# Performance work log

Hardware: AMD Instinct MI355X
Metric: run time of the kernel (lower is better)

The kernel has to match this reference:

```python
import math
import jax, jax.numpy as jnp
import numpy as np

B, LQ, LK = 4, 1024, 1024
D_MODEL, NHEAD, FFN = 1024, 16, 4096
DEPTH = D_MODEL // NHEAD  # 64
MAX_REL = 1024
EPS = 1e-5


def _rel_embedding():
    # fixed (non-learned) buffer: clamped relative-position indices used as float values
    length = max(MAX_REL, DEPTH)
    r = np.arange(length)
    mat = np.clip(r[None, :] - r[:, None], -MAX_REL, MAX_REL) + MAX_REL
    return jnp.asarray(mat[:MAX_REL, :DEPTH], jnp.float32)  # [MAX_REL, DEPTH]


def _skew(rel, length_k):
    # rel: [B, H, Lq, Lq] -> relative logits aligned to key positions [B, H, Lq, Lk]
    b, h, lq, m = rel.shape
    assert lq == m
    rel = jnp.pad(rel, ((0, 0), (0, 0), (0, 0), (1, 0)))
    rel = rel.reshape(b, h, lq + 1, lq)[:, :, 1:, :]
    if length_k > lq:
        rel = jnp.pad(rel, ((0, 0), (0, 0), (0, 0), (0, length_k - lq)))
    elif length_k < lq:
        rel = rel[:, :, :, :length_k]
    return rel


def _split_heads(t):
    b, l, _ = t.shape
    return t.reshape(b, l, NHEAD, DEPTH).transpose(0, 2, 1, 3)  # [b,h,l,d]


def _rga(x_q, x_kv, Wq, bq, Wo, bo, mask, rel_e):
    # NOTE: faithful to source - Q, K and V all use query_projection
    q = _split_heads(x_q @ Wq + bq)
    k = _split_heads(x_kv @ Wq + bq)
    v = _split_heads(x_kv @ Wq + bq)
    lq, lk = q.shape[2], k.shape[2]
    logits = jnp.einsum('bhqd,bhkd->bhqk', q, k)
    start = max(0, MAX_REL - lq)
    ke = rel_e[start:, :]  # [min(MAX_REL,lq), DEPTH]
    rel = jnp.einsum('bhld,md->bhlm', q, ke)
    logits = (logits + _skew(rel, lk)) / math.sqrt(DEPTH)
    if mask is not None:
        logits = jnp.where(mask, logits, jnp.asarray(-1e9, logits.dtype))
    w = jax.nn.softmax(logits, axis=-1)
    out = jnp.einsum('bhqk,bhkd->bhqd', w, v)
    out = out.transpose(0, 2, 1, 3).reshape(x_q.shape[0], lq, D_MODEL)
    return out @ Wo + bo


def _layernorm(x, g, b):
    mu = jnp.mean(x, axis=-1, keepdims=True)
    var = jnp.mean(jnp.square(x - mu), axis=-1, keepdims=True)
    return (x - mu) * jax.lax.rsqrt(var + EPS) * g + b


def setup_inputs() -> dict:
    key = jax.random.key(0)
    ks = jax.random.split(key, 12)
    s = 0.02
    inp = {
        'tgt': jax.random.normal(ks[0], (B, LQ, D_MODEL), jnp.float32),
        'memory': jax.random.normal(ks[1], (B, LK, D_MODEL), jnp.float32),
        'tgt_mask': jnp.tril(jnp.ones((LQ, LQ), dtype=bool)),
        'sa_Wq': jax.random.normal(ks[2], (D_MODEL, D_MODEL), jnp.float32) * s,
        'sa_bq': jnp.zeros((D_MODEL,), jnp.float32),
        'sa_Wo': jax.random.normal(ks[3], (D_MODEL, D_MODEL), jnp.float32) * s,
        'sa_bo': jnp.zeros((D_MODEL,), jnp.float32),
        'ca_Wq': jax.random.normal(ks[4], (D_MODEL, D_MODEL), jnp.float32) * s,
        'ca_bq': jnp.zeros((D_MODEL,), jnp.float32),
        'ca_Wo': jax.random.normal(ks[5], (D_MODEL, D_MODEL), jnp.float32) * s,
        'ca_bo': jnp.zeros((D_MODEL,), jnp.float32),
        'ffn_W1': jax.random.normal(ks[6], (D_MODEL, FFN), jnp.float32) * s,
        'ffn_b1': jnp.zeros((FFN,), jnp.float32),
        'ffn_W2': jax.random.normal(ks[7], (FFN, D_MODEL), jnp.float32) * s,
        'ffn_b2': jnp.zeros((D_MODEL,), jnp.float32),
        'ln1_g': jnp.ones((D_MODEL,), jnp.float32), 'ln1_b': jnp.zeros((D_MODEL,), jnp.float32),
        'ln2_g': jnp.ones((D_MODEL,), jnp.float32), 'ln2_b': jnp.zeros((D_MODEL,), jnp.float32),
        'ln3_g': jnp.ones((D_MODEL,), jnp.float32), 'ln3_b': jnp.zeros((D_MODEL,), jnp.float32),
    }
    return inp


def reference(tgt, memory, tgt_mask, sa_Wq, sa_bq, sa_Wo, sa_bo, ca_Wq, ca_bq, ca_Wo, ca_bo,
              ffn_W1, ffn_b1, ffn_W2, ffn_b2, ln1_g, ln1_b, ln2_g, ln2_b, ln3_g, ln3_b):
    rel_e = _rel_embedding()
    # self-attention (relative-global) with causal mask
    x = tgt + _rga(tgt, tgt, sa_Wq, sa_bq, sa_Wo, sa_bo, tgt_mask, rel_e)
    x = _layernorm(x, ln1_g, ln1_b)
    # cross-attention (also relative-global per source)
    x = x + _rga(x, memory, ca_Wq, ca_bq, ca_Wo, ca_bo, None, rel_e)
    x = _layernorm(x, ln2_g, ln2_b)
    # FFN
    h = jax.nn.relu(x @ ffn_W1 + ffn_b1)
    x = x + (h @ ffn_W2 + ffn_b2)
    x = _layernorm(x, ln3_g, ln3_b)
    return x
```

## Files before the change

kernel.cpp:

```cpp
#include <hip/hip_runtime.h>

typedef __attribute__((ext_vector_type(4))) float f32x4;
typedef __attribute__((ext_vector_type(8))) short s16x8;
typedef __attribute__((ext_vector_type(4))) unsigned short u16x4;

__device__ __forceinline__ unsigned short f2bf(float x) {
  union { float f; unsigned u; } un; un.f = x;
  unsigned u = un.u;
  u += 0x7FFFu + ((u >> 16) & 1u);
  return (unsigned short)(u >> 16);
}
__device__ __forceinline__ float bf2f(unsigned short h) {
  union { unsigned u; float f; } un; un.u = ((unsigned)h) << 16; return un.f;
}

__device__ __forceinline__ f32x4 mfma16(s16x8 a, s16x8 b, f32x4 c) {
  asm("v_mfma_f32_16x16x32_bf16 %0, %1, %2, %0" : "+v"(c) : "v"(a), "v"(b));
  return c;
}

__device__ __forceinline__ void gld16(const void* g, void* l) {
  __builtin_amdgcn_global_load_lds(
      (const __attribute__((address_space(1))) void*)g,
      (__attribute__((address_space(3))) void*)l, 16, 0, 0);
}

template<bool RELU, bool RESID, bool OUT_BF16>
__global__ __launch_bounds__(256, 2) void bgemm_k(
    const unsigned short* __restrict__ Ab, const unsigned short* __restrict__ Bb,
    const float* __restrict__ bias, const float* __restrict__ resid,
    void* __restrict__ Cp, int M, int N, int K, int lbx)
{
  __shared__ __align__(16) unsigned short As[2][128 * 64];
  __shared__ __align__(16) unsigned short Bs[2][128 * 64];

  const int nwg = gridDim.x;
  const int bid = blockIdx.x;
  const int swz = (bid & 7) * (nwg >> 3) + (bid >> 3);
  const int nbx_m1 = (1 << lbx) - 1;
  const int n0 = (swz & nbx_m1) * 128;
  const int m0 = (swz >> lbx) * 128;

  const int tid = threadIdx.x;
  const int lane = tid & 63;
  const int w = tid >> 6;
  const int wm = w >> 1, wn = w & 1;
  const int li = lane & 15, g = lane >> 4;

  f32x4 acc[4][4] = {};

#define STAGE(buf, kt) do { \
    const int k0_ = (kt) * 64; \
    _Pragma("unroll") \
    for (int i_ = 0; i_ < 4; i_++) { \
      int lin = i_ * 256 + tid; int row = lin >> 3; \
      int cg = (lin & 7) ^ (row & 7); \
      gld16(Ab + (size_t)(m0 + row) * K + k0_ + cg * 8, &As[buf][lin * 8]); \
    } \
    _Pragma("unroll") \
    for (int i_ = 0; i_ < 4; i_++) { \
      int lin = i_ * 256 + tid; int row = lin >> 3; \
      int cg = (lin & 7) ^ (row & 7); \
      gld16(Bb + (size_t)(n0 + row) * K + k0_ + cg * 8, &Bs[buf][lin * 8]); \
    } \
  } while (0)

  const int NT = K >> 6;
  STAGE(0, 0);
  for (int t = 0; t < NT; ++t) {
    const int cur = t & 1;
    if (t + 1 < NT) {
      STAGE(cur ^ 1, t + 1);
      asm volatile("s_waitcnt vmcnt(8)" ::: "memory");
    } else {
      asm volatile("s_waitcnt vmcnt(0)" ::: "memory");
    }
    __builtin_amdgcn_sched_barrier(0);
    __builtin_amdgcn_s_barrier();
    __builtin_amdgcn_sched_barrier(0);
#pragma unroll
    for (int ks = 0; ks < 2; ++ks) {
      s16x8 af[4], bf[4];
#pragma unroll
      for (int mt = 0; mt < 4; mt++) {
        int row = wm * 64 + mt * 16 + li;
        int slot = (4 * ks + g) ^ (row & 7);
        af[mt] = *(const s16x8*)&As[cur][row * 64 + slot * 8];
      }
#pragma unroll
      for (int nt = 0; nt < 4; nt++) {
        int row = wn * 64 + nt * 16 + li;
        int slot = (4 * ks + g) ^ (row & 7);
        bf[nt] = *(const s16x8*)&Bs[cur][row * 64 + slot * 8];
      }
#pragma unroll
      for (int mt = 0; mt < 4; mt++)
#pragma unroll
        for (int nt = 0; nt < 4; nt++)
          acc[mt][nt] = mfma16(af[mt], bf[nt], acc[mt][nt]);
    }
    __builtin_amdgcn_sched_barrier(0);
    __builtin_amdgcn_s_barrier();
    __builtin_amdgcn_sched_barrier(0);
  }
#undef STAGE

  asm volatile("s_nop 7\n\ts_nop 7" :::);
#pragma unroll
  for (int mt = 0; mt < 4; mt++) {
    int mrow = m0 + wm * 64 + mt * 16 + 4 * g;
#pragma unroll
    for (int nt = 0; nt < 4; nt++) {
      int ncol = n0 + wn * 64 + nt * 16 + li;
      float bv = bias ? bias[ncol] : 0.f;
#pragma unroll
      for (int r = 0; r < 4; r++) {
        int mr = mrow + r;
        float v = acc[mt][nt][r] + bv;
        if (RESID) v += resid[(size_t)mr * N + ncol];
        if (RELU) v = fmaxf(v, 0.f);
        if (OUT_BF16) ((unsigned short*)Cp)[(size_t)mr * N + ncol] = f2bf(v);
        else          ((float*)Cp)[(size_t)mr * N + ncol] = v;
      }
    }
  }
}

__global__ __launch_bounds__(256, 2) void sgemm_k(
    const unsigned short* __restrict__ Ah, const unsigned short* __restrict__ Al,
    const unsigned short* __restrict__ A2h, const unsigned short* __restrict__ A2l,
    const unsigned short* __restrict__ Bh, const unsigned short* __restrict__ Bl,
    const float* __restrict__ bias,
    unsigned short* __restrict__ Cb, unsigned short* __restrict__ C2b,
    int Ms, int M, int N, int K, int lbx)
{
  __shared__ __align__(16) unsigned short AsH[128 * 64];
  __shared__ __align__(16) unsigned short AsL[128 * 64];
  __shared__ __align__(16) unsigned short BsH[128 * 64];
  __shared__ __align__(16) unsigned short BsL[128 * 64];

  const int nwg = gridDim.x;
  const int bid = blockIdx.x;
  const int swz = (bid & 7) * (nwg >> 3) + (bid >> 3);
  const int nbx_m1 = (1 << lbx) - 1;
  const int n0 = (swz & nbx_m1) * 128;
  int m0 = (swz >> lbx) * 128;

  const unsigned short* Ahp = Ah;
  const unsigned short* Alp = Al;
  unsigned short* Cp = Cb;
  if (m0 >= Ms) { Ahp = A2h; Alp = A2l; Cp = C2b; m0 -= Ms; }

  const int tid = threadIdx.x;
  const int lane = tid & 63;
  const int w = tid >> 6;
  const int wm = w >> 1, wn = w & 1;
  const int li = lane & 15, g = lane >> 4;

  f32x4 acc[4][4] = {};

  const int NT = K >> 6;
  for (int t = 0; t < NT; ++t) {
    __syncthreads();
#pragma unroll
    for (int i = 0; i < 4; i++) {
      int lin = i * 256 + tid; int row = lin >> 3;
      int cg = (lin & 7) ^ (row & 7);
      size_t offA = (size_t)(m0 + row) * K + t * 64 + cg * 8;
      size_t offB = (size_t)(n0 + row) * K + t * 64 + cg * 8;
      gld16(Ahp + offA, &AsH[lin * 8]);
      gld16(Alp + offA, &AsL[lin * 8]);
      gld16(Bh + offB, &BsH[lin * 8]);
      gld16(Bl + offB, &BsL[lin * 8]);
    }
    asm volatile("s_waitcnt vmcnt(0)" ::: "memory");
    __syncthreads();
#pragma unroll
    for (int ks = 0; ks < 2; ++ks) {
      s16x8 ah[4], al[4], bh[4], bl[4];
#pragma unroll
      for (int mt = 0; mt < 4; mt++) {
        int row = wm * 64 + mt * 16 + li;
        int slot = (4 * ks + g) ^ (row & 7);
        ah[mt] = *(const s16x8*)&AsH[row * 64 + slot * 8];
        al[mt] = *(const s16x8*)&AsL[row * 64 + slot * 8];
      }
#pragma unroll
      for (int nt = 0; nt < 4; nt++) {
        int row = wn * 64 + nt * 16 + li;
        int slot = (4 * ks + g) ^ (row & 7);
        bh[nt] = *(const s16x8*)&BsH[row * 64 + slot * 8];
        bl[nt] = *(const s16x8*)&BsL[row * 64 + slot * 8];
      }
#pragma unroll
      for (int mt = 0; mt < 4; mt++)
#pragma unroll
        for (int nt = 0; nt < 4; nt++) {
          acc[mt][nt] = mfma16(ah[mt], bh[nt], acc[mt][nt]);
          acc[mt][nt] = mfma16(ah[mt], bl[nt], acc[mt][nt]);
          acc[mt][nt] = mfma16(al[mt], bh[nt], acc[mt][nt]);
        }
    }
  }

  asm volatile("s_nop 7\n\ts_nop 7" :::);
#pragma unroll
  for (int mt = 0; mt < 4; mt++) {
    int mrow = m0 + wm * 64 + mt * 16 + 4 * g;
#pragma unroll
    for (int nt = 0; nt < 4; nt++) {
      int ncol = n0 + wn * 64 + nt * 16 + li;
      float bv = bias[ncol];
#pragma unroll
      for (int r = 0; r < 4; r++) {
        int mr = mrow + r;
        Cp[(size_t)mr * N + ncol] = f2bf(acc[mt][nt][r] + bv);
      }
    }
  }
}

__device__ __forceinline__ void dev_tc(const float* __restrict__ W,
    unsigned short* __restrict__ WT, int K, int N, int bid, char* ldsu)
{
  unsigned short (*Ls)[65] = (unsigned short (*)[65])ldsu;
  int ntx = N >> 6;
  int ty = bid / ntx, tx = bid - ty * ntx;
  int r0 = ty << 6, c0 = tx << 6;
  int tid = threadIdx.x;
  int rl = tid >> 4, cl = (tid & 15) << 2;
#pragma unroll
  for (int rr = 0; rr < 4; rr++) {
    f32x4 v = *(const f32x4*)&W[(size_t)(r0 + rl + rr * 16) * N + c0 + cl];
#pragma unroll
    for (int j = 0; j < 4; j++) Ls[rl + rr * 16][cl + j] = f2bf(v[j]);
  }
  __syncthreads();
#pragma unroll
  for (int rr = 0; rr < 4; rr++) {
    int nl = rl + rr * 16;
    u16x4 o;
#pragma unroll
    for (int j = 0; j < 4; j++) o[j] = Ls[cl + j][nl];
    *(u16x4*)&WT[(size_t)(c0 + nl) * K + r0 + cl] = o;
  }
}

__device__ __forceinline__ void dev_tc2(const float* __restrict__ W,
    unsigned short* __restrict__ WTh, unsigned short* __restrict__ WTl,
    int K, int N, int bid, char* ldsu)
{
  float (*Ls)[65] = (float (*)[65])ldsu;
  int ntx = N >> 6;
  int ty = bid / ntx, tx = bid - ty * ntx;
  int r0 = ty << 6, c0 = tx << 6;
  int tid = threadIdx.x;
  int rl = tid >> 4, cl = (tid & 15) << 2;
#pragma unroll
  for (int rr = 0; rr < 4; rr++) {
    f32x4 v = *(const f32x4*)&W[(size_t)(r0 + rl + rr * 16) * N + c0 + cl];
#pragma unroll
    for (int j = 0; j < 4; j++) Ls[rl + rr * 16][cl + j] = v[j];
  }
  __syncthreads();
#pragma unroll
  for (int rr = 0; rr < 4; rr++) {
    int nl = rl + rr * 16;
    u16x4 oh, ol;
#pragma unroll
    for (int j = 0; j < 4; j++) {
      float v = Ls[cl + j][nl];
      unsigned short h = f2bf(v);
      oh[j] = h; ol[j] = f2bf(v - bf2f(h));
    }
    *(u16x4*)&WTh[(size_t)(c0 + nl) * K + r0 + cl] = oh;
    *(u16x4*)&WTl[(size_t)(c0 + nl) * K + r0 + cl] = ol;
  }
}

__global__ __launch_bounds__(256) void prep_w_k(
    const float* saWq, const float* caWq, const float* saWo, const float* caWo,
    const float* W1, const float* W2,
    unsigned short* WqTsaH, unsigned short* WqTsaL,
    unsigned short* WqTcaH, unsigned short* WqTcaL,
    unsigned short* WoTsa, unsigned short* WoTca,
    unsigned short* W1T, unsigned short* W2T)
{
  __shared__ __align__(16) char LDSU[64 * 65 * 4];
  int bid = blockIdx.x;
  if (bid < 256)       dev_tc2(saWq, WqTsaH, WqTsaL, 1024, 1024, bid, LDSU);
  else if (bid < 512)  dev_tc2(caWq, WqTcaH, WqTcaL, 1024, 1024, bid - 256, LDSU);
  else if (bid < 768)  dev_tc (saWo, WoTsa, 1024, 1024, bid - 512, LDSU);
  else if (bid < 1024) dev_tc (caWo, WoTca, 1024, 1024, bid - 768, LDSU);
  else if (bid < 2048) dev_tc (W1, W1T, 1024, 4096, bid - 1024, LDSU);
  else                 dev_tc (W2, W2T, 4096, 1024, bid - 2048, LDSU);
}

__device__ __forceinline__ void dev_cvt2row(const float* __restrict__ X,
    unsigned short* __restrict__ H, unsigned short* __restrict__ L, int bid)
{
  int i = (bid * 256 + threadIdx.x) * 4;
  f32x4 v = *(const f32x4*)&X[i];
  u16x4 hh, ll;
#pragma unroll
  for (int j = 0; j < 4; j++) {
    unsigned short h = f2bf(v[j]);
    hh[j] = h; ll[j] = f2bf(v[j] - bf2f(h));
  }
  *(u16x4*)&H[i] = hh;
  *(u16x4*)&L[i] = ll;
}

__device__ __forceinline__ void dev_wrel(const float* __restrict__ Wq,
    float* __restrict__ Wr, int bid)
{
  int idx = bid * 256 + threadIdx.x;
  int k = idx >> 4, h = idx & 15;
  const float* src = Wq + (size_t)k * 1024 + h * 64;
  float a = 0.f, s = 0.f;
#pragma unroll
  for (int d = 0; d < 64; d += 4) {
    f32x4 v = *(const f32x4*)&src[d];
#pragma unroll
    for (int j = 0; j < 4; j++) { a += v[j] * (float)(d + j + 1024); s += v[j]; }
  }
  Wr[k * 32 + h] = a;
  Wr[k * 32 + 16 + h] = s;
}

__device__ __forceinline__ void dev_crel(const float* __restrict__ bq,
    float* __restrict__ cr)
{
  int h = threadIdx.x;
  if (h < 16) {
    float a = 0.f, s = 0.f;
    for (int d = 0; d < 64; d++) { float v = bq[h * 64 + d]; a += v * (float)(d + 1024); s += v; }
    cr[h] = a; cr[16 + h] = s;
  }
}

__global__ __launch_bounds__(256) void prep_a_k(
    const float* tgt, const float* mem,
    unsigned short* tgth, unsigned short* tgtl,
    unsigned short* memh, unsigned short* meml,
    const float* saWq, const float* caWq, float* wrelsa, float* wrelca,
    const float* sabq, const float* cabq, float* crelsa, float* crelca)
{
  int bid = blockIdx.x;
  if (bid < 4096)       dev_cvt2row(tgt, tgth, tgtl, bid);
  else if (bid < 8192)  dev_cvt2row(mem, memh, meml, bid - 4096);
  else if (bid < 8256)  dev_wrel(saWq, wrelsa, bid - 8192);
  else if (bid < 8320)  dev_wrel(caWq, wrelca, bid - 8256);
  else if (bid == 8320) dev_crel(sabq, crelsa);
  else                  dev_crel(cabq, crelca);
}

__global__ __launch_bounds__(256) void relgemm_k(const float* __restrict__ X,
    const float* __restrict__ Wr, const float* __restrict__ cr,
    float* __restrict__ Out)
{
  __shared__ float Xs[8][256];
  __shared__ float Ws[256][32];
  int r0 = blockIdx.x * 8;
  int tid = threadIdx.x;
  int rl = tid >> 5, col = tid & 31;
  float acc = 0.f;
  for (int kc = 0; kc < 1024; kc += 256) {
    __syncthreads();
    {
      const float* xs = X + (size_t)(r0 + rl) * 1024 + kc + col * 8;
      *(f32x4*)&Xs[rl][col * 8] = *(const f32x4*)xs;
      *(f32x4*)&Xs[rl][col * 8 + 4] = *(const f32x4*)(xs + 4);
    }
    {
      const float* wsrc = Wr + (size_t)(kc + tid) * 32;
#pragma unroll
      for (int i = 0; i < 8; i++) *(f32x4*)&Ws[tid][i * 4] = *(const f32x4*)&wsrc[i * 4];
    }
    __syncthreads();
#pragma unroll 8
    for (int kk = 0; kk < 256; ++kk) acc += Xs[rl][kk] * Ws[kk][col];
  }
  Out[(size_t)(r0 + rl) * 32 + col] = acc + cr[col];
}

template<bool CAUSAL>
__global__ __launch_bounds__(512) void attn_k(
    const unsigned short* __restrict__ Qb, const unsigned short* __restrict__ KVb,
    const float* __restrict__ rAS, unsigned short* __restrict__ Ob)
{
  const int bh = blockIdx.x;
  const int b = bh >> 4, h = bh & 15;
  const int y = blockIdx.y;
  const int tid = threadIdx.x, lane = tid & 63, w = tid >> 6;
  const int g = lane >> 4, li = lane & 15;

  __shared__ __align__(16) unsigned short Kt[64 * 64];
  __shared__ __align__(16) unsigned short KT[64 * 64];
  __shared__ __align__(16) unsigned short Pl[8][16 * 64];

  const int tile = CAUSAL ? ((w < 4) ? y : (15 - y)) : (2 * y + (w >> 2));
  const int q0 = tile * 64 + (w & 3) * 16;
  const int nkb = CAUSAL ? (16 - y) : 16;

  s16x8 qf[2];
  {
    const unsigned short* qrow = Qb + (size_t)(b * 1024 + q0 + li) * 1024 + h * 64;
    qf[0] = *(const s16x8*)&qrow[8 * g];
    qf[1] = *(const s16x8*)&qrow[8 * g + 32];
  }
  const float SCL2 = 0.125f * 1.44269504f;
  int qri[4];
  float C0c[4], C1c[4], rSc[4], rS1c[4];
#pragma unroll
  for (int r = 0; r < 4; r++) {
    int qr = q0 + 4 * g + r;
    qri[r] = qr;
    float rA = rAS[(size_t)(b * 1024 + qr) * 32 + h];
    float rS = rAS[(size_t)(b * 1024 + qr) * 32 + 16 + h];
    int q1 = (qr + 1 < 1024) ? qr + 1 : 1023;
    float rA1 = rAS[(size_t)(b * 1024 + q1) * 32 + h];
    float rS1 = rAS[(size_t)(b * 1024 + q1) * 32 + 16 + h];
    C0c[r]  = (rA + (float)(qr - 1023) * rS) * SCL2;
    rSc[r]  = rS * SCL2;
    C1c[r]  = (rA1 + (float)(qr + 2) * rS1) * SCL2;
    rS1c[r] = rS1 * SCL2;
  }

  float mrow[4], lrow[4];
#pragma unroll
  for (int r = 0; r < 4; r++) { mrow[r] = -3.0e38f; lrow[r] = 0.f; }
  f32x4 accO[4] = {};

  for (int kbk = 0; kbk < nkb; kbk++) {
    __syncthreads();
    {
      const unsigned short* src = KVb + (size_t)(b * 1024 + kbk * 64 + lane) * 1024 + h * 64 + w * 8;
      s16x8 v = *(const s16x8*)src;
      int slot = w ^ (lane & 7);
      *(s16x8*)&Kt[lane * 64 + slot * 8] = v;
#pragma unroll
      for (int j = 0; j < 8; j++) {
        int d = w * 8 + j;
        KT[d * 64 + (((lane >> 3) ^ (d & 7)) * 8) + (lane & 7)] = (unsigned short)v[j];
      }
    }
    __syncthreads();
    if (!CAUSAL || kbk <= tile) {
      const bool diag = CAUSAL && (kbk == tile);
      f32x4 accS[4];
#pragma unroll
      for (int nt = 0; nt < 4; nt++) {
        int krow = li + 16 * nt;
        f32x4 c = {};
#pragma unroll
        for (int ks = 0; ks < 2; ks++) {
          int slot = (g + 4 * ks) ^ (krow & 7);
          s16x8 kf = *(const s16x8*)&Kt[krow * 64 + slot * 8];
          c = mfma16(qf[ks], kf, c);
        }
        accS[nt] = c;
      }
      float pv[4][4];
      float bm[4];
#pragma unroll
      for (int r = 0; r < 4; r++) bm[r] = -3.0e38f;
#pragma unroll
      for (int nt = 0; nt < 4; nt++) {
        int kk = kbk * 64 + 16 * nt + li;
        float kkf = (float)kk;
#pragma unroll
        for (int r = 0; r < 4; r++) {
          float sk = (kk <= qri[r]) ? fmaf(kkf, -rSc[r], C0c[r])
                   : ((kk == qri[r] + 1) ? 0.f : fmaf(kkf, -rS1c[r], C1c[r]));
          float lg = fmaf(accS[nt][r], SCL2, sk);
          if (diag && kk > qri[r]) lg = -1.0e9f;
          pv[nt][r] = lg;
          bm[r] = fmaxf(bm[r], lg);
        }
      }
#pragma unroll
      for (int off = 1; off < 16; off <<= 1)
#pragma unroll
        for (int r = 0; r < 4; r++)
          bm[r] = fmaxf(bm[r], __shfl_xor(bm[r], off, 64));
      float scl[4], rsum[4];
#pragma unroll
      for (int r = 0; r < 4; r++) {
        float mnew = fmaxf(mrow[r], bm[r]);
        scl[r] = exp2f(mrow[r] - mnew);
        mrow[r] = mnew;
        rsum[r] = 0.f;
      }
#pragma unroll
      for (int nt = 0; nt < 4; nt++)
#pragma unroll
        for (int r = 0; r < 4; r++) {
          float p = exp2f(pv[nt][r] - mrow[r]);
          pv[nt][r] = p;
          rsum[r] += p;
        }
#pragma unroll
      for (int off = 1; off < 16; off <<= 1)
#pragma unroll
        for (int r = 0; r < 4; r++)
          rsum[r] += __shfl_xor(rsum[r], off, 64);
#pragma unroll
      for (int r = 0; r < 4; r++) lrow[r] = lrow[r] * scl[r] + rsum[r];
#pragma unroll
      for (int nt = 0; nt < 4; nt++)
#pragma unroll
        for (int r = 0; r < 4; r++) {
          int qq = 4 * g + r;
          int kkk = 16 * nt + li;
          int slot = (kkk >> 3) ^ (qq & 7);
          Pl[w][qq * 64 + slot * 8 + (kkk & 7)] = f2bf(pv[nt][r]);
        }
#pragma unroll
      for (int dt = 0; dt < 4; dt++)
#pragma unroll
        for (int r = 0; r < 4; r++) accO[dt][r] *= scl[r];
      s16x8 pfk[2];
#pragma unroll
      for (int ks = 0; ks < 2; ks++) {
        int slotA = (g + 4 * ks) ^ (li & 7);
        pfk[ks] = *(const s16x8*)&Pl[w][li * 64 + slotA * 8];
      }
#pragma unroll
      for (int dt = 0; dt < 4; dt++) {
#pragma unroll
        for (int ks = 0; ks < 2; ks++) {
          int drow = li + 16 * dt;
          int slotB = (g + 4 * ks) ^ (drow & 7);
          s16x8 vf = *(const s16x8*)&KT[drow * 64 + slotB * 8];
          accO[dt] = mfma16(pfk[ks], vf, accO[dt]);
        }
      }
    }
  }
  asm volatile("s_nop 7\n\ts_nop 7" :::);
#pragma unroll
  for (int dt = 0; dt < 4; dt++) {
    int dcol = h * 64 + li + 16 * dt;
#pragma unroll
    for (int r = 0; r < 4; r++) {
      int q = q0 + 4 * g + r;
      Ob[(size_t)(b * 1024 + q) * 1024 + dcol] = f2bf(accO[dt][r] / lrow[r]);
    }
  }
}

__global__ __launch_bounds__(256) void ln_k(const float* __restrict__ X,
    const float* __restrict__ gw, const float* __restrict__ bw,
    float* __restrict__ O, unsigned short* __restrict__ Obh,
    unsigned short* __restrict__ Obl)
{
  int row = blockIdx.x;
  const float* x = X + (size_t)row * 1024;
  int tid = threadIdx.x;
  f32x4 v = *(const f32x4*)&x[tid * 4];
  float s = v[0] + v[1] + v[2] + v[3];
  float s2 = v[0]*v[0] + v[1]*v[1] + v[2]*v[2] + v[3]*v[3];
#pragma unroll
  for (int off = 32; off > 0; off >>= 1) {
    s += __shfl_down(s, off, 64);
    s2 += __shfl_down(s2, off, 64);
  }
  __shared__ float rb[8];
  if ((tid & 63) == 0) { rb[tid >> 6] = s; rb[4 + (tid >> 6)] = s2; }
  __syncthreads();
  float S = rb[0] + rb[1] + rb[2] + rb[3];
  float S2 = rb[4] + rb[5] + rb[6] + rb[7];
  float mu = S * (1.f / 1024.f);
  float var = S2 * (1.f / 1024.f) - mu * mu;
  float rstd = rsqrtf(var + 1e-5f);
  f32x4 go = *(const f32x4*)&gw[tid * 4];
  f32x4 bo = *(const f32x4*)&bw[tid * 4];
  f32x4 r;
#pragma unroll
  for (int j = 0; j < 4; j++) r[j] = (v[j] - mu) * rstd * go[j] + bo[j];
  *(f32x4*)&O[(size_t)row * 1024 + tid * 4] = r;
  if (Obh) {
    u16x4 oh;
#pragma unroll
    for (int j = 0; j < 4; j++) oh[j] = f2bf(r[j]);
    *(u16x4*)&Obh[(size_t)row * 1024 + tid * 4] = oh;
    if (Obl) {
      u16x4 ol;
#pragma unroll
      for (int j = 0; j < 4; j++) ol[j] = f2bf(r[j] - bf2f(f2bf(r[j])));
      *(u16x4*)&Obl[(size_t)row * 1024 + tid * 4] = ol;
    }
  }
}

extern "C" void kernel_launch(void* const* d_in, const int* in_sizes, int n_in,
                              void* d_out, int out_size, void* d_ws, size_t ws_size,
                              hipStream_t stream)
{
  const float* tgt  = (const float*)d_in[0];
  const float* mem  = (const float*)d_in[1];
  const float* saWq = (const float*)d_in[3];
  const float* sabq = (const float*)d_in[4];
  const float* saWo = (const float*)d_in[5];
  const float* sabo = (const float*)d_in[6];
  const float* caWq = (const float*)d_in[7];
  const float* cabq = (const float*)d_in[8];
  const float* caWo = (const float*)d_in[9];
  const float* cabo = (const float*)d_in[10];
  const float* W1   = (const float*)d_in[11];
  const float* b1   = (const float*)d_in[12];
  const float* W2   = (const float*)d_in[13];
  const float* b2   = (const float*)d_in[14];
  const float* g1   = (const float*)d_in[15];
  const float* be1  = (const float*)d_in[16];
  const float* g2   = (const float*)d_in[17];
  const float* be2  = (const float*)d_in[18];
  const float* g3   = (const float*)d_in[19];
  const float* be3  = (const float*)d_in[20];
  float* out = (float*)d_out;

  char* ws = (char*)d_ws;
  const size_t ACT = (size_t)4096 * 1024;
  unsigned short* RA   = (unsigned short*)ws; ws += ACT * 2;
  unsigned short* RB   = (unsigned short*)ws; ws += ACT * 2;
  unsigned short* qkvb = (unsigned short*)ws; ws += ACT * 2;
  unsigned short* kvb  = (unsigned short*)ws; ws += ACT * 2;
  unsigned short* x2b  = (unsigned short*)ws; ws += ACT * 2;
  unsigned short* RF   = (unsigned short*)ws; ws += (size_t)4096 * 4096 * 2;
  unsigned short* memh = RF;
  unsigned short* meml = RF + ACT;
  unsigned short* hb   = RF;
  unsigned short* WqTsaH = (unsigned short*)ws; ws += (size_t)1024 * 1024 * 2;
  unsigned short* WqTsaL = (unsigned short*)ws; ws += (size_t)1024 * 1024 * 2;
  unsigned short* WoTsa  = (unsigned short*)ws; ws += (size_t)1024 * 1024 * 2;
  unsigned short* WqTcaH = (unsigned short*)ws; ws += (size_t)1024 * 1024 * 2;
  unsigned short* WqTcaL = (unsigned short*)ws; ws += (size_t)1024 * 1024 * 2;
  unsigned short* WoTca  = (unsigned short*)ws; ws += (size_t)1024 * 1024 * 2;
  unsigned short* W1T = (unsigned short*)ws; ws += (size_t)4096 * 1024 * 2;
  unsigned short* W2T = (unsigned short*)ws; ws += (size_t)4096 * 1024 * 2;
  float* x2f = (float*)ws; ws += (size_t)4096 * 1024 * 4;
  float* rAS = (float*)ws; ws += (size_t)4096 * 32 * 4;
  float* wrelsa = (float*)ws; ws += (size_t)1024 * 32 * 4;
  float* wrelca = (float*)ws; ws += (size_t)1024 * 32 * 4;
  float* crelsa = (float*)ws; ws += 128;
  float* crelca = (float*)ws; ws += 128;
  float* x1f = out;

  dim3 blk(256);

  prep_w_k<<<dim3(3072), blk, 0, stream>>>(saWq, caWq, saWo, caWo, W1, W2,
      WqTsaH, WqTsaL, WqTcaH, WqTcaL, WoTsa, WoTca, W1T, W2T);
  prep_a_k<<<dim3(8322), blk, 0, stream>>>(tgt, mem, RA, RB, memh, meml,
      saWq, caWq, wrelsa, wrelca, sabq, cabq, crelsa, crelca);

  sgemm_k<<<dim3(256), blk, 0, stream>>>(RA, RB, RA, RB, WqTsaH, WqTsaL, sabq,
      qkvb, qkvb, 1 << 30, 4096, 1024, 1024, 3);
  relgemm_k<<<dim3(512), blk, 0, stream>>>(tgt, wrelsa, crelsa, rAS);
  attn_k<true><<<dim3(64, 8), dim3(512), 0, stream>>>(qkvb, qkvb, rAS, RA);
  bgemm_k<false, true, false><<<dim3(256), blk, 0, stream>>>(RA, WoTsa, sabo, tgt, x1f, 4096, 1024, 1024, 3);
  ln_k<<<dim3(4096), blk, 0, stream>>>(x1f, g1, be1, x1f, RA, RB);
  sgemm_k<<<dim3(512), blk, 0, stream>>>(RA, RB, memh, meml, WqTcaH, WqTcaL, cabq,
      qkvb, kvb, 4096, 8192, 1024, 1024, 3);
  relgemm_k<<<dim3(512), blk, 0, stream>>>(x1f, wrelca, crelca, rAS);
  attn_k<false><<<dim3(64, 8), dim3(512), 0, stream>>>(qkvb, kvb, rAS, RA);
  bgemm_k<false, true, false><<<dim3(256), blk, 0, stream>>>(RA, WoTca, cabo, x1f, x2f, 4096, 1024, 1024, 3);
  ln_k<<<dim3(4096), blk, 0, stream>>>(x2f, g2, be2, x2f, x2b, nullptr);
  bgemm_k<true, false, true><<<dim3(1024), blk, 0, stream>>>(x2b, W1T, b1, nullptr, hb, 4096, 4096, 1024, 5);
  bgemm_k<false, true, false><<<dim3(256), blk, 0, stream>>>(hb, W2T, b2, x2f, out, 4096, 1024, 4096, 3);
  ln_k<<<dim3(4096), blk, 0, stream>>>(out, g3, be3, out, nullptr, nullptr);

  (void)in_sizes; (void)n_in; (void)out_size; (void)ws_size;
}
```

Measured before the change: 481.4 us.

## Double-buffer split-bf16 GEMM LDS tiles with BK=32 prefetch

Restructures the split-precision (hi/lo bf16) projection GEMM kernel to use two LDS buffers with a K-tile of 32 instead of one buffer with a K-tile of 64. The next tile is loaded asynchronously while the current one is multiplied, with a partial vmcnt wait before the barrier. The goal is to hide global-to-LDS load latency behind MFMA work. In exchange it doubles the number of barriers per K element and halves the work per tile. The swizzle also drops to 4 slots, which may raise LDS bank conflicts.

```diff
diff --git a/kernel.cpp b/kernel.cpp
--- a/kernel.cpp
+++ b/kernel.cpp
@@ -134,10 +134,10 @@
     unsigned short* __restrict__ Cb, unsigned short* __restrict__ C2b,
     int Ms, int M, int N, int K, int lbx)
 {
-  __shared__ __align__(16) unsigned short AsH[128 * 64];
-  __shared__ __align__(16) unsigned short AsL[128 * 64];
-  __shared__ __align__(16) unsigned short BsH[128 * 64];
-  __shared__ __align__(16) unsigned short BsL[128 * 64];
+  __shared__ __align__(16) unsigned short AsH[2][128 * 32];
+  __shared__ __align__(16) unsigned short AsL[2][128 * 32];
+  __shared__ __align__(16) unsigned short BsH[2][128 * 32];
+  __shared__ __align__(16) unsigned short BsL[2][128 * 32];
 
   const int nwg = gridDim.x;
   const int bid = blockIdx.x;
@@ -159,38 +159,49 @@
 
   f32x4 acc[4][4] = {};
 
-  const int NT = K >> 6;
+#define SSTAGE(buf, kt) do { \
+    const int k0_ = (kt) * 32; \
+    _Pragma("unroll") \
+    for (int i_ = 0; i_ < 2; i_++) { \
+      int lin = i_ * 256 + tid; int row = lin >> 2; \
+      int cg = (lin & 3) ^ (row & 3); \
+      size_t offA = (size_t)(m0 + row) * K + k0_ + cg * 8; \
+      size_t offB = (size_t)(n0 + row) * K + k0_ + cg * 8; \
+      gld16(Ahp + offA, &AsH[buf][lin * 8]); \
+      gld16(Alp + offA, &AsL[buf][lin * 8]); \
+      gld16(Bh + offB, &BsH[buf][lin * 8]); \
+      gld16(Bl + offB, &BsL[buf][lin * 8]); \
+    } \
+  } while (0)
+
+  const int NT = K >> 5;
+  SSTAGE(0, 0);
   for (int t = 0; t < NT; ++t) {
-    __syncthreads();
-#pragma unroll
-    for (int i = 0; i < 4; i++) {
-      int lin = i * 256 + tid; int row = lin >> 3;
-      int cg = (lin & 7) ^ (row & 7);
-      size_t offA = (size_t)(m0 + row) * K + t * 64 + cg * 8;
-      size_t offB = (size_t)(n0 + row) * K + t * 64 + cg * 8;
-      gld16(Ahp + offA, &AsH[lin * 8]);
-      gld16(Alp + offA, &AsL[lin * 8]);
-      gld16(Bh + offB, &BsH[lin * 8]);
-      gld16(Bl + offB, &BsL[lin * 8]);
-    }
-    asm volatile("s_waitcnt vmcnt(0)" ::: "memory");
-    __syncthreads();
-#pragma unroll
-    for (int ks = 0; ks < 2; ++ks) {
+    const int cur = t & 1;
+    if (t + 1 < NT) {
+      SSTAGE(cur ^ 1, t + 1);
+      asm volatile("s_waitcnt vmcnt(8)" ::: "memory");
+    } else {
+      asm volatile("s_waitcnt vmcnt(0)" ::: "memory");
+    }
+    __builtin_amdgcn_sched_barrier(0);
+    __builtin_amdgcn_s_barrier();
+    __builtin_amdgcn_sched_barrier(0);
+    {
       s16x8 ah[4], al[4], bh[4], bl[4];
 #pragma unroll
       for (int mt = 0; mt < 4; mt++) {
         int row = wm * 64 + mt * 16 + li;
-        int slot = (4 * ks + g) ^ (row & 7);
-        ah[mt] = *(const s16x8*)&AsH[row * 64 + slot * 8];
-        al[mt] = *(const s16x8*)&AsL[row * 64 + slot * 8];
+        int slot = g ^ (row & 3);
+        ah[mt] = *(const s16x8*)&AsH[cur][row * 32 + slot * 8];
+        al[mt] = *(const s16x8*)&AsL[cur][row * 32 + slot * 8];
       }
 #pragma unroll
       for (int nt = 0; nt < 4; nt++) {
         int row = wn * 64 + nt * 16 + li;
-        int slot = (4 * ks + g) ^ (row & 7);
-        bh[nt] = *(const s16x8*)&BsH[row * 64 + slot * 8];
-        bl[nt] = *(const s16x8*)&BsL[row * 64 + slot * 8];
+        int slot = g ^ (row & 3);
+        bh[nt] = *(const s16x8*)&BsH[cur][row * 32 + slot * 8];
+        bl[nt] = *(const s16x8*)&BsL[cur][row * 32 + slot * 8];
       }
 #pragma unroll
       for (int mt = 0; mt < 4; mt++)
@@ -201,7 +212,11 @@
           acc[mt][nt] = mfma16(al[mt], bh[nt], acc[mt][nt]);
         }
     }
-  }
+    __builtin_amdgcn_sched_barrier(0);
+    __builtin_amdgcn_s_barrier();
+    __builtin_amdgcn_sched_barrier(0);
+  }
+#undef SSTAGE
 
   asm volatile("s_nop 7\n\ts_nop 7" :::);
 #pragma unroll
```

Result: slower. 497.1 us (+3.3%).

## Split-K the FFN down-projection GEMM and fuse partial reduction with final layernorm

Applied to the files above, without the earlier changes.

Replaces the single 256-block FFN W2 GEMM (K=4096) with a 2-way split-K kernel launching 512 blocks that write two fp32 partial outputs into reused workspace buffers. A new row kernel sums the partials, adds bias and residual, and applies the final layernorm in one pass, replacing the separate layernorm launch. The aim is better CU occupancy on the 256-CU device, since 256 tiles leave many CUs idle. The cost is an extra write and read of two fp32 4096x1024 partial tensors, and the new layernorm computes variance as E[x^2]-mu^2.

```diff
diff --git a/kernel.cpp b/kernel.cpp
--- a/kernel.cpp
+++ b/kernel.cpp
@@ -126,6 +126,105 @@
   }
 }
 
+__global__ __launch_bounds__(256, 2) void bgemm_pk(
+    const unsigned short* __restrict__ Ab, const unsigned short* __restrict__ Bb,
+    float* __restrict__ P0, float* __restrict__ P1,
+    int M, int N, int K, int KH, int lbx)
+{
+  __shared__ __align__(16) unsigned short As[2][128 * 64];
+  __shared__ __align__(16) unsigned short Bs[2][128 * 64];
+
+  const int nwg = gridDim.x;
+  const int bid = blockIdx.x;
+  const int swz = (bid & 7) * (nwg >> 3) + (bid >> 3);
+  const int nbx_m1 = (1 << lbx) - 1;
+  const int n0 = (swz & nbx_m1) * 128;
+  int m0 = (swz >> lbx) * 128;
+
+  int kb = 0;
+  float* Pp = P0;
+  if (m0 >= M) { m0 -= M; kb = KH; Pp = P1; }
+
+  const int tid = threadIdx.x;
+  const int lane = tid & 63;
+  const int w = tid >> 6;
+  const int wm = w >> 1, wn = w & 1;
+  const int li = lane & 15, g = lane >> 4;
+
+  f32x4 acc[4][4] = {};
+
+#define PSTAGE(buf, kt) do { \
+    const int k0_ = kb + (kt) * 64; \
+    _Pragma("unroll") \
+    for (int i_ = 0; i_ < 4; i_++) { \
+      int lin = i_ * 256 + tid; int row = lin >> 3; \
+      int cg = (lin & 7) ^ (row & 7); \
+      gld16(Ab + (size_t)(m0 + row) * K + k0_ + cg * 8, &As[buf][lin * 8]); \
+    } \
+    _Pragma("unroll") \
+    for (int i_ = 0; i_ < 4; i_++) { \
+      int lin = i_ * 256 + tid; int row = lin >> 3; \
+      int cg = (lin & 7) ^ (row & 7); \
+      gld16(Bb + (size_t)(n0 + row) * K + k0_ + cg * 8, &Bs[buf][lin * 8]); \
+    } \
+  } while (0)
+
+  const int NT = KH >> 6;
+  PSTAGE(0, 0);
+  for (int t = 0; t < NT; ++t) {
+    const int cur = t & 1;
+    if (t + 1 < NT) {
+      PSTAGE(cur ^ 1, t + 1);
+      asm volatile("s_waitcnt vmcnt(8)" ::: "memory");
+    } else {
+      asm volatile("s_waitcnt vmcnt(0)" ::: "memory");
+    }
+    __builtin_amdgcn_sched_barrier(0);
+    __builtin_amdgcn_s_barrier();
+    __builtin_amdgcn_sched_barrier(0);
+#pragma unroll
+    for (int ks = 0; ks < 2; ++ks) {
+      s16x8 af[4], bf[4];
+#pragma unroll
+      for (int mt = 0; mt < 4; mt++) {
+        int row = wm * 64 + mt * 16 + li;
+        int slot = (4 * ks + g) ^ (row & 7);
+        af[mt] = *(const s16x8*)&As[cur][row * 64 + slot * 8];
+      }
+#pragma unroll
+      for (int nt = 0; nt < 4; nt++) {
+        int row = wn * 64 + nt * 16 + li;
+        int slot = (4 * ks + g) ^ (row & 7);
+        bf[nt] = *(const s16x8*)&Bs[cur][row * 64 + slot * 8];
+      }
+#pragma unroll
+      for (int mt = 0; mt < 4; mt++)
+#pragma unroll
+        for (int nt = 0; nt < 4; nt++)
+          acc[mt][nt] = mfma16(af[mt], bf[nt], acc[mt][nt]);
+    }
+    __builtin_amdgcn_sched_barrier(0);
+    __builtin_amdgcn_s_barrier();
+    __builtin_amdgcn_sched_barrier(0);
+  }
+#undef PSTAGE
+
+  asm volatile("s_nop 7\n\ts_nop 7" :::);
+#pragma unroll
+  for (int mt = 0; mt < 4; mt++) {
+    int mrow = m0 + wm * 64 + mt * 16 + 4 * g;
+#pragma unroll
+    for (int nt = 0; nt < 4; nt++) {
+      int ncol = n0 + wn * 64 + nt * 16 + li;
+#pragma unroll
+      for (int r = 0; r < 4; r++) {
+        int mr = mrow + r;
+        Pp[(size_t)mr * N + ncol] = acc[mt][nt][r];
+      }
+    }
+  }
+}
+
 __global__ __launch_bounds__(256, 2) void sgemm_k(
     const unsigned short* __restrict__ Ah, const unsigned short* __restrict__ Al,
     const unsigned short* __restrict__ A2h, const unsigned short* __restrict__ A2l,
@@ -592,6 +691,45 @@
       *(u16x4*)&Obl[(size_t)row * 1024 + tid * 4] = ol;
     }
   }
+}
+
+__global__ __launch_bounds__(256) void redln_k(
+    const float* __restrict__ P0, const float* __restrict__ P1,
+    const float* __restrict__ bias, const float* __restrict__ resid,
+    const float* __restrict__ gw, const float* __restrict__ bw,
+    float* __restrict__ O)
+{
+  int row = blockIdx.x;
+  int tid = threadIdx.x;
+  size_t base = (size_t)row * 1024 + tid * 4;
+  f32x4 a = *(const f32x4*)&P0[base];
+  f32x4 b = *(const f32x4*)&P1[base];
+  f32x4 c = *(const f32x4*)&resid[base];
+  f32x4 bv = *(const f32x4*)&bias[tid * 4];
+  f32x4 v;
+#pragma unroll
+  for (int j = 0; j < 4; j++) v[j] = a[j] + b[j] + bv[j] + c[j];
+  float s = v[0] + v[1] + v[2] + v[3];
+  float s2 = v[0]*v[0] + v[1]*v[1] + v[2]*v[2] + v[3]*v[3];
+#pragma unroll
+  for (int off = 32; off > 0; off >>= 1) {
+    s += __shfl_down(s, off, 64);
+    s2 += __shfl_down(s2, off, 64);
+  }
+  __shared__ float rb[8];
+  if ((tid & 63) == 0) { rb[tid >> 6] = s; rb[4 + (tid >> 6)] = s2; }
+  __syncthreads();
+  float S = rb[0] + rb[1] + rb[2] + rb[3];
+  float S2 = rb[4] + rb[5] + rb[6] + rb[7];
+  float mu = S * (1.f / 1024.f);
+  float var = S2 * (1.f / 1024.f) - mu * mu;
+  float rstd = rsqrtf(var + 1e-5f);
+  f32x4 go = *(const f32x4*)&gw[tid * 4];
+  f32x4 bo = *(const f32x4*)&bw[tid * 4];
+  f32x4 r;
+#pragma unroll
+  for (int j = 0; j < 4; j++) r[j] = (v[j] - mu) * rstd * go[j] + bo[j];
+  *(f32x4*)&O[base] = r;
 }
 
 extern "C" void kernel_launch(void* const* d_in, const int* in_sizes, int n_in,
@@ -631,6 +769,8 @@
   unsigned short* memh = RF;
   unsigned short* meml = RF + ACT;
   unsigned short* hb   = RF;
+  float* P0 = (float*)qkvb;
+  float* P1 = (float*)RA;
   unsigned short* WqTsaH = (unsigned short*)ws; ws += (size_t)1024 * 1024 * 2;
   unsigned short* WqTsaL = (unsigned short*)ws; ws += (size_t)1024 * 1024 * 2;
   unsigned short* WoTsa  = (unsigned short*)ws; ws += (size_t)1024 * 1024 * 2;
@@ -667,8 +807,8 @@
   bgemm_k<false, true, false><<<dim3(256), blk, 0, stream>>>(RA, WoTca, cabo, x1f, x2f, 4096, 1024, 1024, 3);
   ln_k<<<dim3(4096), blk, 0, stream>>>(x2f, g2, be2, x2f, x2b, nullptr);
   bgemm_k<true, false, true><<<dim3(1024), blk, 0, stream>>>(x2b, W1T, b1, nullptr, hb, 4096, 4096, 1024, 5);
-  bgemm_k<false, true, false><<<dim3(256), blk, 0, stream>>>(hb, W2T, b2, x2f, out, 4096, 1024, 4096, 3);
-  ln_k<<<dim3(4096), blk, 0, stream>>>(out, g3, be3, out, nullptr, nullptr);
+  bgemm_pk<<<dim3(512), blk, 0, stream>>>(hb, W2T, P0, P1, 4096, 1024, 4096, 2048, 3);
+  redln_k<<<dim3(4096), blk, 0, stream>>>(P0, P1, b2, x2f, g3, be3, out);
 
   (void)in_sizes; (void)n_in; (void)out_size; (void)ws_size;
 }
```

After: 459.2 us. 4.6% less time.
